# Optimization experiments

Measured on AMD Instinct MI355X. Metric: run time of the kernel, lower is better.

The kernel has to match this reference:

```python
import jax, jax.numpy as jnp
import numpy as np

B, N, D = 32, 1024, 256  # batch, nodes, feature dim (input=hidden=output=256)


def setup_inputs() -> dict:
    key = jax.random.key(0)
    ks = jax.random.split(key, 9)
    x = jax.random.normal(ks[0], (B, N, D), dtype=jnp.float32)
    # binary node mask (multiplied in, so float dtype)
    mask = (jax.random.uniform(ks[1], (B, N)) > 0.2).astype(jnp.float32)
    # dense nonneg adjacency; row sums > 0 almost surely
    adj = jax.random.uniform(ks[2], (B, N, N), dtype=jnp.float32)
    s = 1.0 / np.sqrt(D)
    W0 = jax.random.normal(ks[3], (D, D), dtype=jnp.float32) * s
    b0 = jnp.zeros((D,), dtype=jnp.float32)
    W1 = jax.random.normal(ks[4], (D, D), dtype=jnp.float32) * s
    b1 = jnp.zeros((D,), dtype=jnp.float32)
    W2 = jax.random.normal(ks[5], (D, D), dtype=jnp.float32) * s
    b2 = jnp.zeros((D,), dtype=jnp.float32)
    return {"x": x, "mask": mask, "adj": adj,
            "W0": W0, "b0": b0, "W1": W1, "b1": b1, "W2": W2, "b2": b2}


def reference(x, mask, adj, W0, b0, W1, b1, W2, b2):
    # D_hat = diag(1/rowsum(adj)) with inf -> 0; diag matmul == row-wise scale
    deg = jnp.sum(adj, axis=-1)                                   # [B,N]
    dinv = jnp.where(deg != 0, 1.0 / jnp.where(deg != 0, deg, 1.0), 0.0)
    adj_n = adj * dinv[..., None]                                 # [B,N,N]
    xm = mask[..., None]                                          # [B,N,1]
    # dropout is identity in eval mode
    for W, b in ((W0, b0), (W1, b1), (W2, b2)):
        x = jnp.matmul(x, W.T) + b                                # linear
        x = jnp.einsum('bnm,bmd->bnd', adj_n, x)                  # aggregate
        x = x * xm                                                # mask
        x = jax.nn.gelu(x, approximate=False)                     # exact gelu (torch F.gelu)
    return x
```

## Files before the change

### kernel.cpp

```cpp
#include <hip/hip_runtime.h>
#include <stdint.h>


typedef __attribute__((ext_vector_type(8))) short short8;
typedef __attribute__((ext_vector_type(4))) float f32x4;

__device__ __forceinline__ uint16_t f2bf(float f) {
  uint32_t u = __float_as_uint(f);
  u += 0x7FFF + ((u >> 16) & 1);
  return (uint16_t)(u >> 16);
}
__device__ __forceinline__ float bf2f(uint16_t h) {
  return __uint_as_float(((uint32_t)h) << 16);
}
__device__ __forceinline__ float gelu_exact(float v) {
  return 0.5f * v * (1.0f + erff(v * 0.70710678118654752f));
}
__device__ __forceinline__ f32x4 mfma16(short8 a, short8 b, f32x4 c) {
  return __builtin_amdgcn_mfma_f32_16x16x32_bf16(a, b, c, 0, 0, 0);
}

#define GLD16(gsrc, ldst) __builtin_amdgcn_global_load_lds(                    \
    (const __attribute__((address_space(1))) void*)(gsrc),                     \
    (__attribute__((address_space(3))) void*)(ldst), 16, 0, 0)

__global__ void k_split(const float* __restrict__ src, uint16_t* __restrict__ h,
                        uint16_t* __restrict__ l, int n4) {
  int i = blockIdx.x * blockDim.x + threadIdx.x;
  if (i >= n4) return;
  const float4 v = ((const float4*)src)[i];
  float vv[4] = {v.x, v.y, v.z, v.w};
  ushort4 hh, ll;
  uint16_t* hp = (uint16_t*)&hh;
  uint16_t* lp = (uint16_t*)&ll;
#pragma unroll
  for (int e = 0; e < 4; ++e) {
    uint16_t hb = f2bf(vv[e]);
    hp[e] = hb;
    lp[e] = f2bf(vv[e] - bf2f(hb));
  }
  ((ushort4*)h)[i] = hh;
  ((ushort4*)l)[i] = ll;
}

__global__ void k_norm_adj(const float* __restrict__ adj, uint16_t* __restrict__ An) {
  const int r = blockIdx.x;
  const int t = threadIdx.x;
  const float* row = adj + (size_t)r * 1024;
  const float4 v = *(const float4*)(row + t * 4);
  float s = v.x + v.y + v.z + v.w;
#pragma unroll
  for (int off = 32; off; off >>= 1) s += __shfl_down(s, off);
  __shared__ float ws[4];
  if ((t & 63) == 0) ws[t >> 6] = s;
  __syncthreads();
  const float deg = ws[0] + ws[1] + ws[2] + ws[3];
  const float dinv = (deg != 0.f) ? 1.f / deg : 0.f;
  ushort4 o;
  uint16_t* op = (uint16_t*)&o;
  float vv[4] = {v.x, v.y, v.z, v.w};
#pragma unroll
  for (int e = 0; e < 4; ++e) op[e] = f2bf(vv[e] * dinv);
  const int b = r >> 10, node = r & 1023;
  const int mb = node >> 7, rr = node & 127;
  const int kt = t >> 3, ko = (t * 4) & 31;
  const size_t oo = (size_t)(b * 8 + mb) * 131072 + kt * 4096 + rr * 32 + ko;
  *(ushort4*)(An + oo) = o;
}

__global__ __launch_bounds__(256) void k_linear(
    const uint16_t* __restrict__ Xh, const uint16_t* __restrict__ Xl,
    const uint16_t* __restrict__ Wh, const uint16_t* __restrict__ Wl,
    const float* __restrict__ bias,
    uint16_t* __restrict__ Yth) {
  __shared__ __align__(16) uint8_t smem[32768];
  const int tid = threadIdx.x;
  const int lane = tid & 63;
  const int wave = tid >> 6;
  const int wr = wave >> 1, wc = wave & 1;
  const int m0 = blockIdx.x * 128;
  const int n0 = blockIdx.y * 128;
  const int lm = lane & 15, g = lane >> 4;
  const int srow = lane >> 2;
  const int skof = (lane & 3) * 8;

  f32x4 acc[4][4] = {};

  for (int kt = 0; kt < 8; ++kt) {
    const int k0 = kt * 32;
    __syncthreads();
#pragma unroll
    for (int j = 0; j < 8; ++j) {
      const int c = j * 4 + wave;
      const int sub = c & 7, which = c >> 3;
      const int row = sub * 16 + srow;
      const uint16_t* src;
      if (which == 0)      src = Xh + (size_t)(m0 + row) * 256 + k0 + skof;
      else if (which == 1) src = Xl + (size_t)(m0 + row) * 256 + k0 + skof;
      else if (which == 2) src = Wh + (size_t)(n0 + row) * 256 + k0 + skof;
      else                 src = Wl + (size_t)(n0 + row) * 256 + k0 + skof;
      GLD16(src, smem + c * 1024);
    }
    asm volatile("s_waitcnt vmcnt(0)" ::: "memory");
    __syncthreads();

    const uint8_t* Ahs = smem;
    const uint8_t* Als = smem + 8192;
    const uint8_t* Bhs = smem + 16384;
    const uint8_t* Bls = smem + 24576;
    short8 ah[4], al[4], bh[4], bl[4];
#pragma unroll
    for (int f = 0; f < 4; ++f) {
      ah[f] = *(const short8*)(Ahs + (wr * 64 + f * 16 + lm) * 64 + g * 16);
      al[f] = *(const short8*)(Als + (wr * 64 + f * 16 + lm) * 64 + g * 16);
      bh[f] = *(const short8*)(Bhs + (wc * 64 + f * 16 + lm) * 64 + g * 16);
      bl[f] = *(const short8*)(Bls + (wc * 64 + f * 16 + lm) * 64 + g * 16);
    }
#pragma unroll
    for (int fm = 0; fm < 4; ++fm)
#pragma unroll
      for (int fn = 0; fn < 4; ++fn) {
        acc[fm][fn] = mfma16(ah[fm], bh[fn], acc[fm][fn]);
        acc[fm][fn] = mfma16(ah[fm], bl[fn], acc[fm][fn]);
        acc[fm][fn] = mfma16(al[fm], bh[fn], acc[fm][fn]);
      }
  }

#pragma unroll
  for (int fn = 0; fn < 4; ++fn) {
    const int n = n0 + wc * 64 + fn * 16 + lm;
    const float bv = bias[n];
#pragma unroll
    for (int fm = 0; fm < 4; ++fm) {
      const int mg = m0 + wr * 64 + fm * 16 + g * 4;
      const int bb = mg >> 10, node = mg & 1023;
      const int kt = node >> 5, ko = node & 31;
      ushort4 hh;
      uint16_t* hp = (uint16_t*)&hh;
#pragma unroll
      for (int e = 0; e < 4; ++e) hp[e] = f2bf(acc[fm][fn][e] + bv);
      const size_t o = ((size_t)(bb * 32 + kt) * 256 + n) * 32 + ko;
      *(ushort4*)(Yth + o) = hh;
    }
  }
}

#define STAGE(T, SSL) {                                                        \
    const size_t ta_ = (size_t)(T) * 4096;                                     \
    const size_t tb_ = (size_t)(T) * 8192;                                     \
    uint8_t* d_ = smem + (SSL) + wofs;                                         \
    GLD16(gA + ta_,        d_);                                                \
    GLD16(gH + tb_,        d_ + 8192);                                         \
    GLD16(gH + tb_ + 4096, d_ + 16384);                                        \
  }

template <bool LAST>
__global__ __launch_bounds__(512, 1) void k_agg(
    const uint16_t* __restrict__ An,
    const uint16_t* __restrict__ Yth,
    const float* __restrict__ mask,
    uint16_t* __restrict__ Xh, uint16_t* __restrict__ Xl,
    float* __restrict__ out) {
  __shared__ __align__(16) uint8_t smem[98304];
  const int tid = threadIdx.x;
  const int lane = tid & 63;
  const int wave = tid >> 6;
  const int wr = wave >> 2, wc = wave & 3;
  const int id = blockIdx.x;
  const int swz = (id & 7) * 32 + (id >> 3);
  const int b = swz >> 3;
  const int mb = swz & 7;
  const int lm = lane & 15, g = lane >> 4;
  const int wofs = wave * 1024;

  const uint16_t* gA = An  + (size_t)(b * 8 + mb) * 131072 + tid * 8;
  const uint16_t* gH = Yth + (size_t)b * 262144 + tid * 8;

  const int aoff = (wr * 64 + lm) * 64 + g * 16;
  const int boff = (wc * 64 + lm) * 64 + g * 16;

  f32x4 acc[4][4] = {};

  STAGE(0, 0);
  STAGE(1, 24576);
  STAGE(2, 49152);

  int csl = 0, ssl = 73728;
#pragma unroll 1
  for (int t = 0; t < 32; ++t) {
    if (t <= 29)      { asm volatile("s_waitcnt vmcnt(6)" ::: "memory"); }
    else if (t == 30) { asm volatile("s_waitcnt vmcnt(3)" ::: "memory"); }
    else              { asm volatile("s_waitcnt vmcnt(0)" ::: "memory"); }
    __builtin_amdgcn_s_barrier();
    __builtin_amdgcn_sched_barrier(0);
    if (t < 29) { STAGE(t + 3, ssl); }
    __builtin_amdgcn_sched_barrier(0);

    const uint8_t* sb = smem + csl;
    short8 af[4], hf[4];
#pragma unroll
    for (int f = 0; f < 4; ++f) {
      af[f] = *(const short8*)(sb + aoff + f * 1024);
      hf[f] = *(const short8*)(sb + 8192 + boff + f * 1024);
    }
    __builtin_amdgcn_s_setprio(1);
#pragma unroll
    for (int fm = 0; fm < 4; ++fm)
#pragma unroll
      for (int fn = 0; fn < 4; ++fn)
        acc[fm][fn] = mfma16(af[fm], hf[fn], acc[fm][fn]);
    __builtin_amdgcn_s_setprio(0);

    csl += 24576; if (csl == 98304) csl = 0;
    ssl += 24576; if (ssl == 98304) ssl = 0;
  }

  const float* mk_b = mask + b * 1024;
#pragma unroll
  for (int fm = 0; fm < 4; ++fm) {
    const int m = mb * 128 + wr * 64 + fm * 16 + g * 4;
    float mk[4];
#pragma unroll
    for (int e = 0; e < 4; ++e) mk[e] = mk_b[m + e];
#pragma unroll
    for (int fn = 0; fn < 4; ++fn) {
      const int n = wc * 64 + fn * 16 + lm;
#pragma unroll
      for (int e = 0; e < 4; ++e) {
        const float v = gelu_exact(acc[fm][fn][e] * mk[e]);
        const size_t o = ((size_t)(b * 1024 + m + e)) * 256 + n;
        if (LAST) {
          out[o] = v;
        } else {
          const uint16_t hb = f2bf(v);
          Xh[o] = hb;
          Xl[o] = f2bf(v - bf2f(hb));
        }
      }
    }
  }
}

extern "C" void kernel_launch(void* const* d_in, const int* in_sizes, int n_in,
                              void* d_out, int out_size, void* d_ws, size_t ws_size,
                              hipStream_t stream) {
  const float* x    = (const float*)d_in[0];
  const float* mask = (const float*)d_in[1];
  const float* adj  = (const float*)d_in[2];
  const float* W[3]  = {(const float*)d_in[3], (const float*)d_in[5], (const float*)d_in[7]};
  const float* bs[3] = {(const float*)d_in[4], (const float*)d_in[6], (const float*)d_in[8]};

  uint8_t* ws = (uint8_t*)d_ws;
  uint16_t* An  = (uint16_t*)(ws);
  uint16_t* Xh  = (uint16_t*)(ws + 67108864);
  uint16_t* Xl  = (uint16_t*)(ws + 83886080);
  uint16_t* Yth = (uint16_t*)(ws + 100663296);
  uint16_t* Wh  = (uint16_t*)(ws + 134217728);
  uint16_t* Wl  = (uint16_t*)(ws + 134610944);

  k_split<<<dim3(8192), 256, 0, stream>>>(x, Xh, Xl, 2097152);
  for (int i = 0; i < 3; ++i)
    k_split<<<dim3(64), 256, 0, stream>>>(W[i], Wh + i * 65536, Wl + i * 65536, 16384);
  k_norm_adj<<<dim3(32768), 256, 0, stream>>>(adj, An);

  for (int l = 0; l < 3; ++l) {
    k_linear<<<dim3(256, 2), 256, 0, stream>>>(Xh, Xl, Wh + l * 65536, Wl + l * 65536,
                                               bs[l], Yth);
    if (l < 2)
      k_agg<false><<<dim3(256), 512, 0, stream>>>(An, Yth, mask, Xh, Xl, nullptr);
    else
      k_agg<true><<<dim3(256), 512, 0, stream>>>(An, Yth, mask, nullptr, nullptr,
                                                 (float*)d_out);
  }
}
```

Before: 211.4 us.

## Restructure aggregation to per-wave 16-row strips with register-staged Y double buffering

Reworks the aggregation kernel so each wave owns a 16-row by 256-column output strip. The A fragments now load straight from global memory into registers, while the Y tiles go through registers into a double-buffered 128KB LDS, four k-tiles per chunk. This replaces the 4-stage global_load_lds pipeline and the 2x4 wave grid that needed LDS reads of both A and Y. The aim is fewer LDS reads for A and larger chunks per barrier, at the cost of more register pressure, uncoalesced A loads and less overlap from the shallower pipeline.

Measured after the change: 281.4 us. +33.1%, slower.

```diff
diff --git a/kernel.cpp b/kernel.cpp
--- a/kernel.cpp
+++ b/kernel.cpp
@@ -145,15 +145,6 @@
   }
 }
 
-#define STAGE(T, SSL) {                                                        \
-    const size_t ta_ = (size_t)(T) * 4096;                                     \
-    const size_t tb_ = (size_t)(T) * 8192;                                     \
-    uint8_t* d_ = smem + (SSL) + wofs;                                         \
-    GLD16(gA + ta_,        d_);                                                \
-    GLD16(gH + tb_,        d_ + 8192);                                         \
-    GLD16(gH + tb_ + 4096, d_ + 16384);                                        \
-  }
-
 template <bool LAST>
 __global__ __launch_bounds__(512, 1) void k_agg(
     const uint16_t* __restrict__ An,
@@ -161,81 +152,87 @@
     const float* __restrict__ mask,
     uint16_t* __restrict__ Xh, uint16_t* __restrict__ Xl,
     float* __restrict__ out) {
-  __shared__ __align__(16) uint8_t smem[98304];
+  __shared__ __align__(16) uint8_t smem[131072];
   const int tid = threadIdx.x;
   const int lane = tid & 63;
-  const int wave = tid >> 6;
-  const int wr = wave >> 2, wc = wave & 3;
+  const int w = tid >> 6;
   const int id = blockIdx.x;
   const int swz = (id & 7) * 32 + (id >> 3);
   const int b = swz >> 3;
   const int mb = swz & 7;
   const int lm = lane & 15, g = lane >> 4;
-  const int wofs = wave * 1024;
-
-  const uint16_t* gA = An  + (size_t)(b * 8 + mb) * 131072 + tid * 8;
-  const uint16_t* gH = Yth + (size_t)b * 262144 + tid * 8;
-
-  const int aoff = (wr * 64 + lm) * 64 + g * 16;
-  const int boff = (wc * 64 + lm) * 64 + g * 16;
-
-  f32x4 acc[4][4] = {};
-
-  STAGE(0, 0);
-  STAGE(1, 24576);
-  STAGE(2, 49152);
-
-  int csl = 0, ssl = 73728;
+
+  const uint16_t* gA = An  + (size_t)(b * 8 + mb) * 131072;
+  const uint16_t* gH = Yth + (size_t)b * 262144;
+  const uint16_t* aSrc = gA + (w * 16 + lm) * 32 + g * 8;
+  const uint16_t* ySrc = gH + tid * 8;
+
+  f32x4 acc[16] = {};
+  int4 y[8];
+
+#pragma unroll
+  for (int j = 0; j < 8; ++j) y[j] = *(const int4*)(ySrc + j * 4096);
+#pragma unroll
+  for (int j = 0; j < 8; ++j) *(int4*)(smem + j * 8192 + tid * 16) = y[j];
+
 #pragma unroll 1
-  for (int t = 0; t < 32; ++t) {
-    if (t <= 29)      { asm volatile("s_waitcnt vmcnt(6)" ::: "memory"); }
-    else if (t == 30) { asm volatile("s_waitcnt vmcnt(3)" ::: "memory"); }
-    else              { asm volatile("s_waitcnt vmcnt(0)" ::: "memory"); }
+  for (int c = 0; c < 8; ++c) {
+    asm volatile("s_waitcnt lgkmcnt(0)" ::: "memory");
+    __builtin_amdgcn_sched_barrier(0);
     __builtin_amdgcn_s_barrier();
+    const uint8_t* rbuf = smem + (c & 1) * 65536;
+    uint8_t* wbuf = smem + ((c + 1) & 1) * 65536;
+
+    short8 af0 = *(const short8*)(aSrc + (size_t)(4 * c + 0) * 4096);
+    short8 af1 = *(const short8*)(aSrc + (size_t)(4 * c + 1) * 4096);
+    short8 af2 = *(const short8*)(aSrc + (size_t)(4 * c + 2) * 4096);
+    short8 af3 = *(const short8*)(aSrc + (size_t)(4 * c + 3) * 4096);
     __builtin_amdgcn_sched_barrier(0);
-    if (t < 29) { STAGE(t + 3, ssl); }
+    if (c < 7) {
+#pragma unroll
+      for (int j = 0; j < 8; ++j)
+        y[j] = *(const int4*)(ySrc + (size_t)(c + 1) * 32768 + j * 4096);
+    }
     __builtin_amdgcn_sched_barrier(0);
 
-    const uint8_t* sb = smem + csl;
-    short8 af[4], hf[4];
-#pragma unroll
-    for (int f = 0; f < 4; ++f) {
-      af[f] = *(const short8*)(sb + aoff + f * 1024);
-      hf[f] = *(const short8*)(sb + 8192 + boff + f * 1024);
-    }
-    __builtin_amdgcn_s_setprio(1);
-#pragma unroll
-    for (int fm = 0; fm < 4; ++fm)
-#pragma unroll
-      for (int fn = 0; fn < 4; ++fn)
-        acc[fm][fn] = mfma16(af[fm], hf[fn], acc[fm][fn]);
-    __builtin_amdgcn_s_setprio(0);
-
-    csl += 24576; if (csl == 98304) csl = 0;
-    ssl += 24576; if (ssl == 98304) ssl = 0;
+#pragma unroll
+    for (int i = 0; i < 4; ++i) {
+      const uint8_t* kb = rbuf + i * 16384;
+      const short8 afi = (i == 0) ? af0 : (i == 1) ? af1 : (i == 2) ? af2 : af3;
+      __builtin_amdgcn_s_setprio(1);
+#pragma unroll
+      for (int fn = 0; fn < 16; ++fn) {
+        const short8 hf = *(const short8*)(kb + (fn * 16 + lm) * 64 + g * 16);
+        acc[fn] = mfma16(afi, hf, acc[fn]);
+      }
+      __builtin_amdgcn_s_setprio(0);
+    }
+
+    if (c < 7) {
+      __builtin_amdgcn_sched_barrier(0);
+#pragma unroll
+      for (int j = 0; j < 8; ++j) *(int4*)(wbuf + j * 8192 + tid * 16) = y[j];
+    }
   }
 
   const float* mk_b = mask + b * 1024;
-#pragma unroll
-  for (int fm = 0; fm < 4; ++fm) {
-    const int m = mb * 128 + wr * 64 + fm * 16 + g * 4;
-    float mk[4];
-#pragma unroll
-    for (int e = 0; e < 4; ++e) mk[e] = mk_b[m + e];
-#pragma unroll
-    for (int fn = 0; fn < 4; ++fn) {
-      const int n = wc * 64 + fn * 16 + lm;
-#pragma unroll
-      for (int e = 0; e < 4; ++e) {
-        const float v = gelu_exact(acc[fm][fn][e] * mk[e]);
-        const size_t o = ((size_t)(b * 1024 + m + e)) * 256 + n;
-        if (LAST) {
-          out[o] = v;
-        } else {
-          const uint16_t hb = f2bf(v);
-          Xh[o] = hb;
-          Xl[o] = f2bf(v - bf2f(hb));
-        }
+  const int m_base = mb * 128 + w * 16 + g * 4;
+  float mk[4];
+#pragma unroll
+  for (int e = 0; e < 4; ++e) mk[e] = mk_b[m_base + e];
+#pragma unroll
+  for (int fn = 0; fn < 16; ++fn) {
+    const int n = fn * 16 + lm;
+#pragma unroll
+    for (int e = 0; e < 4; ++e) {
+      const float v = gelu_exact(acc[fn][e] * mk[e]);
+      const size_t o = ((size_t)(b * 1024 + m_base + e)) * 256 + n;
+      if (LAST) {
+        out[o] = v;
+      } else {
+        const uint16_t hb = f2bf(v);
+        Xh[o] = hb;
+        Xl[o] = f2bf(v - bf2f(hb));
       }
     }
   }
```

## Retile aggregation kernel to 64-row tiles with 4 waves and two blocks per CU

Applied to the files above, without the earlier changes.

The aggregation GEMM moves from 128x256 tiles with 8 waves per block to 64x256 tiles with 4 waves, launching 512 blocks with 2 per CU. The LDS ring drops from four stages to three, cutting shared memory so two blocks fit per CU. Each wave now computes a 32x128 sub-tile, loading B fragments inside the MFMA loop. The aim is better occupancy and latency hiding across blocks, at the cost of reloading the Y tile twice as often and a shallower prefetch depth.

Result: faster. 202.5 us (-4.2%).

```diff
diff --git a/kernel.cpp b/kernel.cpp
--- a/kernel.cpp
+++ b/kernel.cpp
@@ -146,85 +146,83 @@
 }
 
 #define STAGE(T, SSL) {                                                        \
-    const size_t ta_ = (size_t)(T) * 4096;                                     \
-    const size_t tb_ = (size_t)(T) * 8192;                                     \
-    uint8_t* d_ = smem + (SSL) + wofs;                                         \
-    GLD16(gA + ta_,        d_);                                                \
-    GLD16(gH + tb_,        d_ + 8192);                                         \
-    GLD16(gH + tb_ + 4096, d_ + 16384);                                        \
+    _Pragma("unroll")                                                          \
+    for (int j = 0; j < 5; ++j) {                                              \
+      const int c = w * 5 + j;                                                 \
+      const uint16_t* src = (c < 4)                                            \
+          ? aStep + (size_t)(T) * 4096 + c * 512                               \
+          : yStep + (size_t)(T) * 8192 + (c - 4) * 512;                        \
+      GLD16(src, smem + (SSL) + c * 1024);                                     \
+    }                                                                          \
   }
 
 template <bool LAST>
-__global__ __launch_bounds__(512, 1) void k_agg(
+__global__ __launch_bounds__(256, 2) void k_agg(
     const uint16_t* __restrict__ An,
     const uint16_t* __restrict__ Yth,
     const float* __restrict__ mask,
     uint16_t* __restrict__ Xh, uint16_t* __restrict__ Xl,
     float* __restrict__ out) {
-  __shared__ __align__(16) uint8_t smem[98304];
+  __shared__ __align__(16) uint8_t smem[61440];
   const int tid = threadIdx.x;
   const int lane = tid & 63;
-  const int wave = tid >> 6;
-  const int wr = wave >> 2, wc = wave & 3;
+  const int w = tid >> 6;
+  const int wm = w >> 1, wn = w & 1;
   const int id = blockIdx.x;
-  const int swz = (id & 7) * 32 + (id >> 3);
-  const int b = swz >> 3;
-  const int mb = swz & 7;
+  const int swz = (id & 7) * 64 + (id >> 3);
+  const int b = swz >> 4;
+  const int mb2 = swz & 15;
   const int lm = lane & 15, g = lane >> 4;
-  const int wofs = wave * 1024;
-
-  const uint16_t* gA = An  + (size_t)(b * 8 + mb) * 131072 + tid * 8;
-  const uint16_t* gH = Yth + (size_t)b * 262144 + tid * 8;
-
-  const int aoff = (wr * 64 + lm) * 64 + g * 16;
-  const int boff = (wc * 64 + lm) * 64 + g * 16;
-
-  f32x4 acc[4][4] = {};
+
+  const uint16_t* aStep = An + (size_t)(b * 8 + (mb2 >> 1)) * 131072
+                             + (mb2 & 1) * 2048 + lane * 8;
+  const uint16_t* yStep = Yth + (size_t)b * 262144 + lane * 8;
+
+  const int aoff = (wm * 32 + lm) * 64 + g * 16;
+  const int boff = 4096 + (wn * 128 + lm) * 64 + g * 16;
+
+  f32x4 acc[2][8] = {};
 
   STAGE(0, 0);
-  STAGE(1, 24576);
-  STAGE(2, 49152);
-
-  int csl = 0, ssl = 73728;
+  STAGE(1, 20480);
+
+  int csl = 0, ssl = 40960;
 #pragma unroll 1
   for (int t = 0; t < 32; ++t) {
-    if (t <= 29)      { asm volatile("s_waitcnt vmcnt(6)" ::: "memory"); }
-    else if (t == 30) { asm volatile("s_waitcnt vmcnt(3)" ::: "memory"); }
-    else              { asm volatile("s_waitcnt vmcnt(0)" ::: "memory"); }
+    if (t < 31) { asm volatile("s_waitcnt vmcnt(5)" ::: "memory"); }
+    else        { asm volatile("s_waitcnt vmcnt(0)" ::: "memory"); }
     __builtin_amdgcn_s_barrier();
     __builtin_amdgcn_sched_barrier(0);
-    if (t < 29) { STAGE(t + 3, ssl); }
+    if (t < 30) { STAGE(t + 2, ssl); }
     __builtin_amdgcn_sched_barrier(0);
 
     const uint8_t* sb = smem + csl;
-    short8 af[4], hf[4];
-#pragma unroll
-    for (int f = 0; f < 4; ++f) {
-      af[f] = *(const short8*)(sb + aoff + f * 1024);
-      hf[f] = *(const short8*)(sb + 8192 + boff + f * 1024);
-    }
+    const short8 af0 = *(const short8*)(sb + aoff);
+    const short8 af1 = *(const short8*)(sb + aoff + 1024);
     __builtin_amdgcn_s_setprio(1);
 #pragma unroll
-    for (int fm = 0; fm < 4; ++fm)
-#pragma unroll
-      for (int fn = 0; fn < 4; ++fn)
-        acc[fm][fn] = mfma16(af[fm], hf[fn], acc[fm][fn]);
+    for (int fn = 0; fn < 8; ++fn) {
+      const short8 hf = *(const short8*)(sb + boff + fn * 1024);
+      acc[0][fn] = mfma16(af0, hf, acc[0][fn]);
+      acc[1][fn] = mfma16(af1, hf, acc[1][fn]);
+    }
     __builtin_amdgcn_s_setprio(0);
 
-    csl += 24576; if (csl == 98304) csl = 0;
-    ssl += 24576; if (ssl == 98304) ssl = 0;
+    csl += 20480; if (csl == 61440) csl = 0;
+    ssl += 20480; if (ssl == 61440) ssl = 0;
   }
 
   const float* mk_b = mask + b * 1024;
-#pragma unroll
-  for (int fm = 0; fm < 4; ++fm) {
-    const int m = mb * 128 + wr * 64 + fm * 16 + g * 4;
+  const int m0 = mb2 * 64 + wm * 32;
+#pragma unroll
+  for (int fm = 0; fm < 2; ++fm) {
+    const int m = m0 + fm * 16 + g * 4;
     float mk[4];
 #pragma unroll
     for (int e = 0; e < 4; ++e) mk[e] = mk_b[m + e];
 #pragma unroll
-    for (int fn = 0; fn < 4; ++fn) {
-      const int n = wc * 64 + fn * 16 + lm;
+    for (int fn = 0; fn < 8; ++fn) {
+      const int n = wn * 128 + fn * 16 + lm;
 #pragma unroll
       for (int e = 0; e < 4; ++e) {
         const float v = gelu_exact(acc[fm][fn][e] * mk[e]);
@@ -267,9 +265,9 @@
     k_linear<<<dim3(256, 2), 256, 0, stream>>>(Xh, Xl, Wh + l * 65536, Wl + l * 65536,
                                                bs[l], Yth);
     if (l < 2)
-      k_agg<false><<<dim3(256), 512, 0, stream>>>(An, Yth, mask, Xh, Xl, nullptr);
+      k_agg<false><<<dim3(512), 256, 0, stream>>>(An, Yth, mask, Xh, Xl, nullptr);
     else
-      k_agg<true><<<dim3(256), 512, 0, stream>>>(An, Yth, mask, nullptr, nullptr,
+      k_agg<true><<<dim3(512), 256, 0, stream>>>(An, Yth, mask, nullptr, nullptr,
                                                  (float*)d_out);
   }
 }
```
